# Performance work log

Measured on AMD Instinct MI355X. Metric: run time of the kernel, lower is better.

## Reference

```python
import jax, jax.numpy as jnp
import numpy as np

D_K = 32  # hard-coded in original module


def setup_inputs() -> dict:
    key = jax.random.key(0)
    kq, kk, kv, km = jax.random.split(key, 4)
    B, H, S, D = 4, 12, 2048, D_K
    Q = jax.random.normal(kq, (B, H, S, D), dtype=jnp.float32)
    K = jax.random.normal(kk, (B, H, S, D), dtype=jnp.float32)
    V = jax.random.normal(kv, (B, H, S, D), dtype=jnp.float32)
    attn_mask = jax.random.bernoulli(km, 0.5, (B, H, S, S))
    return {"Q": Q, "K": K, "V": V, "attn_mask": attn_mask}


def tanh_max(a):
    # (exp(a) - exp(-a)) / sum_over_keys(exp(a) + exp(-a))
    ea = jnp.exp(a)
    ena = jnp.exp(-a)
    return (ea - ena) / (ea + ena).sum(axis=-1, keepdims=True)


def reference(Q, K, V, attn_mask):
    # scores: [B,H,S,S]
    scores = jnp.einsum("bhqd,bhkd->bhqk", Q, K) / np.sqrt(D_K).astype(np.float32)
    attn = tanh_max(scores)
    # NOTE: original calls attn.masked_fill(attn_mask, 0.0) WITHOUT assignment
    # (non-in-place), so the mask has no effect. Reproduced faithfully.
    context = jnp.einsum("bhqk,bhkd->bhqd", attn, V)
    return context
```

## Files before the change

kernel.cpp:

```cpp
#include <hip/hip_runtime.h>
#include <hip/hip_bf16.h>
#include <cstdint>
#include <cstddef>


#define SLEN 2048
#define DK   32
#define NBH  48
#define PROW 40
#define NCH  32

typedef __attribute__((ext_vector_type(8))) short bf16x8;
typedef __attribute__((ext_vector_type(4))) float f32x4;

__device__ __forceinline__ unsigned pk2(float a, float b) {
    __hip_bfloat162 h = __float22bfloat162_rn(make_float2(a, b));
    union { __hip_bfloat162 h2; unsigned u; } cv; cv.h2 = h; return cv.u;
}

__global__ __launch_bounds__(256)
void prep_kv(const float* __restrict__ K, const float* __restrict__ V,
             unsigned short* __restrict__ Kbf, unsigned short* __restrict__ VTf) {
    if (blockIdx.x < NBH * 32) {
        const int b  = blockIdx.x;
        const int bh = b >> 5, kg = b & 31;
        const int tl = threadIdx.x >> 6, l = threadIdx.x & 63;
        const int t  = kg * 4 + tl;
        const int c  = t >> 1, tb = t & 1;
        const int key = c * 32 + 2 * (l & 15) + tb;
        const float* src = K + ((size_t)bh * SLEN + key) * DK + (l >> 4) * 8;
        float4 a = *(const float4*)src;
        float4 b4 = *(const float4*)(src + 4);
        union { uint4 q; unsigned u[4]; } o;
        o.u[0] = pk2(a.x, a.y);  o.u[1] = pk2(a.z, a.w);
        o.u[2] = pk2(b4.x, b4.y); o.u[3] = pk2(b4.z, b4.w);
        *(uint4*)(Kbf + (((size_t)bh * 128 + t) * 64 + l) * 8) = o.q;
    } else {
        __shared__ float tile[32][33];
        const int b  = blockIdx.x - NBH * 32;
        const int bh = b >> 6, c = b & 63;
        const int t  = threadIdx.x;
        {
            const int row = t >> 3, c4 = (t & 7) * 4;
            float4 v4 = *(const float4*)(V + ((size_t)bh * SLEN + c * 32 + row) * DK + c4);
            tile[row][c4 + 0] = v4.x; tile[row][c4 + 1] = v4.y;
            tile[row][c4 + 2] = v4.z; tile[row][c4 + 3] = v4.w;
        }
        __syncthreads();
        const int h = t >> 7, l = (t >> 1) & 63, jh = t & 1;
        const int col = h * 16 + (l & 15);
        const int r0  = (l >> 4) * 8 + jh * 4;
        uint2 u;
        u.x = pk2(tile[r0 + 0][col], tile[r0 + 1][col]);
        u.y = pk2(tile[r0 + 2][col], tile[r0 + 3][col]);
        *(uint2*)(VTf + ((((size_t)bh * 64 + c) * 2 + h) * 64 + l) * 8 + jh * 4) = u;
    }
}

__global__ __launch_bounds__(256, 4)
void attn_mfma(const float* __restrict__ Q, const unsigned short* __restrict__ Kbf,
               const unsigned short* __restrict__ VTf, float* __restrict__ Out) {
    __shared__ __align__(16) unsigned short Pbuf[4][32 * PROW];
    __shared__ __align__(16) float Red[2][64][24];

    const int tid  = threadIdx.x;
    const int lane = tid & 63;
    const int wv   = tid >> 6;
    const int quad = lane >> 4;
    const int l16  = lane & 15;
    const int qi   = wv >> 1;
    const int kh   = wv & 1;

    const int b   = blockIdx.x;
    const int xcd = b & 7;
    const int i   = b >> 3;
    const int bh  = xcd * 6 + (i % 6);
    const int j   = i / 6;
    const int qbase = (j * 2 + qi) * 32;

    const float sc = 0.17677669529663687f * 1.4426950408889634f;
    union { bf16x8 v; unsigned u[4]; } aQ0, aQ1;
    {
        const float* qp0 = Q + ((size_t)bh * SLEN + qbase + l16) * DK + quad * 8;
        float4 qa = *(const float4*)qp0;
        float4 qb = *(const float4*)(qp0 + 4);
        aQ0.u[0] = pk2(qa.x * sc, qa.y * sc); aQ0.u[1] = pk2(qa.z * sc, qa.w * sc);
        aQ0.u[2] = pk2(qb.x * sc, qb.y * sc); aQ0.u[3] = pk2(qb.z * sc, qb.w * sc);
        const float* qp1 = qp0 + 16 * DK;
        float4 qc = *(const float4*)qp1;
        float4 qd = *(const float4*)(qp1 + 4);
        aQ1.u[0] = pk2(qc.x * sc, qc.y * sc); aQ1.u[1] = pk2(qc.z * sc, qc.w * sc);
        aQ1.u[2] = pk2(qd.x * sc, qd.y * sc); aQ1.u[3] = pk2(qd.z * sc, qd.w * sc);
    }

    const bf16x8* kf = (const bf16x8*)Kbf + ((size_t)bh * 128 + kh * 64) * 64 + lane;
    const bf16x8* vf = (const bf16x8*)VTf + ((size_t)bh * 128 + kh * 64) * 64 + lane;

    f32x4 o00 = {0,0,0,0}, o01 = {0,0,0,0};
    f32x4 o10 = {0,0,0,0}, o11 = {0,0,0,0};
    f32x4 den0 = {0,0,0,0}, den1 = {0,0,0,0};
    const f32x4 zero = {0,0,0,0};

    unsigned short* pb  = &Pbuf[wv][0];
    unsigned*       pbw = (unsigned*)pb;

    bf16x8 k0 = kf[0], k1 = kf[64];

    for (int c = 0; c < NCH; ++c) {
        f32x4 s00 = __builtin_amdgcn_mfma_f32_16x16x32_bf16(aQ0.v, k0, zero, 0, 0, 0);
        f32x4 s01 = __builtin_amdgcn_mfma_f32_16x16x32_bf16(aQ0.v, k1, zero, 0, 0, 0);
        f32x4 s10 = __builtin_amdgcn_mfma_f32_16x16x32_bf16(aQ1.v, k0, zero, 0, 0, 0);
        f32x4 s11 = __builtin_amdgcn_mfma_f32_16x16x32_bf16(aQ1.v, k1, zero, 0, 0, 0);

        bf16x8 v0 = vf[(size_t)c * 128];
        bf16x8 v1 = vf[(size_t)c * 128 + 64];
        const int cn = (c + 1) & (NCH - 1);
        k0 = kf[(size_t)cn * 128];
        k1 = kf[(size_t)cn * 128 + 64];

        #pragma unroll
        for (int r = 0; r < 4; ++r) {
            float e0  = __builtin_amdgcn_exp2f(s00[r]);
            float en0 = __builtin_amdgcn_exp2f(-s00[r]);
            float e1  = __builtin_amdgcn_exp2f(s01[r]);
            float en1 = __builtin_amdgcn_exp2f(-s01[r]);
            den0[r] += (e0 + en0) + (e1 + en1);
            pbw[(quad * 4 + r) * (PROW / 2) + l16] = pk2(e0 - en0, e1 - en1);
        }
        #pragma unroll
        for (int r = 0; r < 4; ++r) {
            float e0  = __builtin_amdgcn_exp2f(s10[r]);
            float en0 = __builtin_amdgcn_exp2f(-s10[r]);
            float e1  = __builtin_amdgcn_exp2f(s11[r]);
            float en1 = __builtin_amdgcn_exp2f(-s11[r]);
            den1[r] += (e0 + en0) + (e1 + en1);
            pbw[(16 + quad * 4 + r) * (PROW / 2) + l16] = pk2(e0 - en0, e1 - en1);
        }

        bf16x8 aP0 = *(const bf16x8*)(pb + l16 * PROW + quad * 8);
        bf16x8 aP1 = *(const bf16x8*)(pb + (16 + l16) * PROW + quad * 8);

        o00 = __builtin_amdgcn_mfma_f32_16x16x32_bf16(aP0, v0, o00, 0, 0, 0);
        o01 = __builtin_amdgcn_mfma_f32_16x16x32_bf16(aP0, v1, o01, 0, 0, 0);
        o10 = __builtin_amdgcn_mfma_f32_16x16x32_bf16(aP1, v0, o10, 0, 0, 0);
        o11 = __builtin_amdgcn_mfma_f32_16x16x32_bf16(aP1, v1, o11, 0, 0, 0);
    }

    #pragma unroll
    for (int r = 0; r < 4; ++r) {
        den0[r] += __shfl_xor(den0[r], 1, 16);
        den0[r] += __shfl_xor(den0[r], 2, 16);
        den0[r] += __shfl_xor(den0[r], 4, 16);
        den0[r] += __shfl_xor(den0[r], 8, 16);
        den1[r] += __shfl_xor(den1[r], 1, 16);
        den1[r] += __shfl_xor(den1[r], 2, 16);
        den1[r] += __shfl_xor(den1[r], 4, 16);
        den1[r] += __shfl_xor(den1[r], 8, 16);
    }

    if (kh == 1) {
        float* r = &Red[qi][lane][0];
        *(f32x4*)(r +  0) = o00; *(f32x4*)(r +  4) = o01;
        *(f32x4*)(r +  8) = o10; *(f32x4*)(r + 12) = o11;
        *(f32x4*)(r + 16) = den0; *(f32x4*)(r + 20) = den1;
    }
    __syncthreads();
    if (kh == 0) {
        const float* r = &Red[qi][lane][0];
        o00 += *(const f32x4*)(r +  0); o01 += *(const f32x4*)(r +  4);
        o10 += *(const f32x4*)(r +  8); o11 += *(const f32x4*)(r + 12);
        den0 += *(const f32x4*)(r + 16); den1 += *(const f32x4*)(r + 20);

        float* outp = Out + ((size_t)bh * SLEN + qbase) * DK;
        #pragma unroll
        for (int rr = 0; rr < 4; ++rr) {
            float inv0 = 1.0f / den0[rr];
            float inv1 = 1.0f / den1[rr];
            int q0 = quad * 4 + rr;
            int q1 = 16 + quad * 4 + rr;
            outp[(size_t)q0 * DK + l16]      = o00[rr] * inv0;
            outp[(size_t)q0 * DK + 16 + l16] = o01[rr] * inv0;
            outp[(size_t)q1 * DK + l16]      = o10[rr] * inv1;
            outp[(size_t)q1 * DK + 16 + l16] = o11[rr] * inv1;
        }
    }
}

extern "C" void kernel_launch(void* const* d_in, const int* in_sizes, int n_in,
                              void* d_out, int out_size, void* d_ws, size_t ws_size,
                              hipStream_t stream) {
    const float* Q = (const float*)d_in[0];
    const float* K = (const float*)d_in[1];
    const float* V = (const float*)d_in[2];
    float* Out = (float*)d_out;
    unsigned short* Kbf = (unsigned short*)d_ws;
    unsigned short* VTf = Kbf + (size_t)NBH * SLEN * DK;

    prep_kv<<<dim3(NBH * 32 + NBH * 64), dim3(256), 0, stream>>>(K, V, Kbf, VTf);
    attn_mfma<<<dim3(1536), dim3(256), 0, stream>>>(Q, Kbf, VTf, Out);
}
```

Measured before the change: 926.9 us.

## Keep P in registers by computing transposed scores and permuting K layout

Swaps the MFMA operand order so the score tile comes out transposed, and permutes the key order in the prepacked K buffer so each lane's score outputs directly form the A-operand fragment for the P·V MFMA. This removes the per-chunk LDS write and read of the P tile along with its shared buffer. The denominator becomes a per-lane scalar reduced across quads, with a width-16 shuffle at the end to redistribute it per row. The scheme depends on the key permutation matching the MFMA register layout exactly, or results will be wrong.

```diff
diff --git a/kernel.cpp b/kernel.cpp
--- a/kernel.cpp
+++ b/kernel.cpp
@@ -7,7 +7,6 @@
 #define SLEN 2048
 #define DK   32
 #define NBH  48
-#define PROW 40
 #define NCH  32
 
 typedef __attribute__((ext_vector_type(8))) short bf16x8;
@@ -25,16 +24,17 @@
         const int b  = blockIdx.x;
         const int bh = b >> 5, kg = b & 31;
         const int tl = threadIdx.x >> 6, l = threadIdx.x & 63;
-        const int t  = kg * 4 + tl;
-        const int c  = t >> 1, tb = t & 1;
-        const int key = c * 32 + 2 * (l & 15) + tb;
+        const int T  = kg * 4 + tl;
+        const int c  = T >> 1, tb = T & 1;
+        const int l16 = l & 15;
+        const int key = c * 32 + 8 * (l16 >> 2) + 2 * (l16 & 3) + tb;
         const float* src = K + ((size_t)bh * SLEN + key) * DK + (l >> 4) * 8;
         float4 a = *(const float4*)src;
         float4 b4 = *(const float4*)(src + 4);
         union { uint4 q; unsigned u[4]; } o;
         o.u[0] = pk2(a.x, a.y);  o.u[1] = pk2(a.z, a.w);
         o.u[2] = pk2(b4.x, b4.y); o.u[3] = pk2(b4.z, b4.w);
-        *(uint4*)(Kbf + (((size_t)bh * 128 + t) * 64 + l) * 8) = o.q;
+        *(uint4*)(Kbf + (((size_t)bh * 128 + T) * 64 + l) * 8) = o.q;
     } else {
         __shared__ float tile[32][33];
         const int b  = blockIdx.x - NBH * 32;
@@ -60,8 +60,7 @@
 __global__ __launch_bounds__(256, 4)
 void attn_mfma(const float* __restrict__ Q, const unsigned short* __restrict__ Kbf,
                const unsigned short* __restrict__ VTf, float* __restrict__ Out) {
-    __shared__ __align__(16) unsigned short Pbuf[4][32 * PROW];
-    __shared__ __align__(16) float Red[2][64][24];
+    __shared__ __align__(16) float Red[2][64][20];
 
     const int tid  = threadIdx.x;
     const int lane = tid & 63;
@@ -98,19 +97,16 @@
 
     f32x4 o00 = {0,0,0,0}, o01 = {0,0,0,0};
     f32x4 o10 = {0,0,0,0}, o11 = {0,0,0,0};
-    f32x4 den0 = {0,0,0,0}, den1 = {0,0,0,0};
+    float den0 = 0.f, den1 = 0.f;
     const f32x4 zero = {0,0,0,0};
-
-    unsigned short* pb  = &Pbuf[wv][0];
-    unsigned*       pbw = (unsigned*)pb;
 
     bf16x8 k0 = kf[0], k1 = kf[64];
 
     for (int c = 0; c < NCH; ++c) {
-        f32x4 s00 = __builtin_amdgcn_mfma_f32_16x16x32_bf16(aQ0.v, k0, zero, 0, 0, 0);
-        f32x4 s01 = __builtin_amdgcn_mfma_f32_16x16x32_bf16(aQ0.v, k1, zero, 0, 0, 0);
-        f32x4 s10 = __builtin_amdgcn_mfma_f32_16x16x32_bf16(aQ1.v, k0, zero, 0, 0, 0);
-        f32x4 s11 = __builtin_amdgcn_mfma_f32_16x16x32_bf16(aQ1.v, k1, zero, 0, 0, 0);
+        f32x4 s00 = __builtin_amdgcn_mfma_f32_16x16x32_bf16(k0, aQ0.v, zero, 0, 0, 0);
+        f32x4 s01 = __builtin_amdgcn_mfma_f32_16x16x32_bf16(k1, aQ0.v, zero, 0, 0, 0);
+        f32x4 s10 = __builtin_amdgcn_mfma_f32_16x16x32_bf16(k0, aQ1.v, zero, 0, 0, 0);
+        f32x4 s11 = __builtin_amdgcn_mfma_f32_16x16x32_bf16(k1, aQ1.v, zero, 0, 0, 0);
 
         bf16x8 v0 = vf[(size_t)c * 128];
         bf16x8 v1 = vf[(size_t)c * 128 + 64];
@@ -118,14 +114,15 @@
         k0 = kf[(size_t)cn * 128];
         k1 = kf[(size_t)cn * 128 + 64];
 
+        union { bf16x8 v; unsigned u[4]; } aP0, aP1;
         #pragma unroll
         for (int r = 0; r < 4; ++r) {
             float e0  = __builtin_amdgcn_exp2f(s00[r]);
             float en0 = __builtin_amdgcn_exp2f(-s00[r]);
             float e1  = __builtin_amdgcn_exp2f(s01[r]);
             float en1 = __builtin_amdgcn_exp2f(-s01[r]);
-            den0[r] += (e0 + en0) + (e1 + en1);
-            pbw[(quad * 4 + r) * (PROW / 2) + l16] = pk2(e0 - en0, e1 - en1);
+            den0 += (e0 + en0) + (e1 + en1);
+            aP0.u[r] = pk2(e0 - en0, e1 - en1);
         }
         #pragma unroll
         for (int r = 0; r < 4; ++r) {
@@ -133,49 +130,37 @@
             float en0 = __builtin_amdgcn_exp2f(-s10[r]);
             float e1  = __builtin_amdgcn_exp2f(s11[r]);
             float en1 = __builtin_amdgcn_exp2f(-s11[r]);
-            den1[r] += (e0 + en0) + (e1 + en1);
-            pbw[(16 + quad * 4 + r) * (PROW / 2) + l16] = pk2(e0 - en0, e1 - en1);
+            den1 += (e0 + en0) + (e1 + en1);
+            aP1.u[r] = pk2(e0 - en0, e1 - en1);
         }
 
-        bf16x8 aP0 = *(const bf16x8*)(pb + l16 * PROW + quad * 8);
-        bf16x8 aP1 = *(const bf16x8*)(pb + (16 + l16) * PROW + quad * 8);
-
-        o00 = __builtin_amdgcn_mfma_f32_16x16x32_bf16(aP0, v0, o00, 0, 0, 0);
-        o01 = __builtin_amdgcn_mfma_f32_16x16x32_bf16(aP0, v1, o01, 0, 0, 0);
-        o10 = __builtin_amdgcn_mfma_f32_16x16x32_bf16(aP1, v0, o10, 0, 0, 0);
-        o11 = __builtin_amdgcn_mfma_f32_16x16x32_bf16(aP1, v1, o11, 0, 0, 0);
+        o00 = __builtin_amdgcn_mfma_f32_16x16x32_bf16(aP0.v, v0, o00, 0, 0, 0);
+        o01 = __builtin_amdgcn_mfma_f32_16x16x32_bf16(aP0.v, v1, o01, 0, 0, 0);
+        o10 = __builtin_amdgcn_mfma_f32_16x16x32_bf16(aP1.v, v0, o10, 0, 0, 0);
+        o11 = __builtin_amdgcn_mfma_f32_16x16x32_bf16(aP1.v, v1, o11, 0, 0, 0);
     }
 
-    #pragma unroll
-    for (int r = 0; r < 4; ++r) {
-        den0[r] += __shfl_xor(den0[r], 1, 16);
-        den0[r] += __shfl_xor(den0[r], 2, 16);
-        den0[r] += __shfl_xor(den0[r], 4, 16);
-        den0[r] += __shfl_xor(den0[r], 8, 16);
-        den1[r] += __shfl_xor(den1[r], 1, 16);
-        den1[r] += __shfl_xor(den1[r], 2, 16);
-        den1[r] += __shfl_xor(den1[r], 4, 16);
-        den1[r] += __shfl_xor(den1[r], 8, 16);
-    }
+    den0 += __shfl_xor(den0, 16); den0 += __shfl_xor(den0, 32);
+    den1 += __shfl_xor(den1, 16); den1 += __shfl_xor(den1, 32);
 
     if (kh == 1) {
         float* r = &Red[qi][lane][0];
         *(f32x4*)(r +  0) = o00; *(f32x4*)(r +  4) = o01;
         *(f32x4*)(r +  8) = o10; *(f32x4*)(r + 12) = o11;
-        *(f32x4*)(r + 16) = den0; *(f32x4*)(r + 20) = den1;
+        r[16] = den0; r[17] = den1;
     }
     __syncthreads();
     if (kh == 0) {
         const float* r = &Red[qi][lane][0];
         o00 += *(const f32x4*)(r +  0); o01 += *(const f32x4*)(r +  4);
         o10 += *(const f32x4*)(r +  8); o11 += *(const f32x4*)(r + 12);
-        den0 += *(const f32x4*)(r + 16); den1 += *(const f32x4*)(r + 20);
+        den0 += r[16]; den1 += r[17];
 
         float* outp = Out + ((size_t)bh * SLEN + qbase) * DK;
         #pragma unroll
         for (int rr = 0; rr < 4; ++rr) {
-            float inv0 = 1.0f / den0[rr];
-            float inv1 = 1.0f / den1[rr];
+            float inv0 = 1.0f / __shfl(den0, quad * 4 + rr, 16);
+            float inv1 = 1.0f / __shfl(den1, quad * 4 + rr, 16);
             int q0 = quad * 4 + rr;
             int q1 = 16 + quad * 4 + rr;
             outp[(size_t)q0 * DK + l16]      = o00[rr] * inv0;
```

Measured after the change: 926.6 us. No clear change (-0.0%).
